# Performance work log

Measured on AMD Instinct MI355X. Metric: run time of the kernel, lower is better.

The kernel has to match this reference:

```python
import jax, jax.numpy as jnp
import numpy as np

N_QUBITS = 8
DEPTH = 2
DIM = 2 ** N_QUBITS

# Hadamard gate (symmetric)
_H = (1.0 / np.sqrt(2.0)) * jnp.array([[1.0, 1.0], [1.0, -1.0]], dtype=jnp.complex64)
# sign table for <Z_i>: bit of wire i is bit (n-1-i) of the basis index (wire 0 = MSB)
_bits = (np.arange(DIM)[:, None] >> np.arange(N_QUBITS - 1, -1, -1)[None, :]) & 1
_SIGNS = jnp.asarray(1.0 - 2.0 * _bits, dtype=jnp.float32)  # [DIM, n_qubits]


def _quantum(ang):
    """Vectorized statevector simulation of the circuit:
    RX(ang_i) on each wire, then DEPTH x (CNOT ladder + H on last wire);
    returns <Z_i> for each wire. ang: [R, N_QUBITS] float32 -> [R, N_QUBITS]."""
    R = ang.shape[0]
    half = ang * 0.5
    a0 = jnp.cos(half).astype(jnp.complex64)
    a1 = (jnp.sin(half) * (-1j)).astype(jnp.complex64)  # RX|0> = cos|0> - i sin|1>
    single = jnp.stack([a0, a1], axis=-1)  # [R, n, 2]
    # product state via kron over qubits (wire 0 is the most significant factor)
    state = single[:, 0]  # [R, 2]
    for q in range(1, N_QUBITS):
        state = (state[:, :, None] * single[:, q][:, None, :]).reshape(R, -1)
    for _ in range(DEPTH):
        # CNOT ladder on adjacent wires (i -> i+1)
        for i in range(N_QUBITS - 1):
            s = state.reshape(R, 2 ** i, 2, 2, -1)  # [R, pre, ctrl, tgt, post]
            s = jnp.concatenate([s[:, :, :1], s[:, :, 1:, ::-1]], axis=2)
            state = s.reshape(R, -1)
        # Hadamard on the last wire
        s = state.reshape(R, -1, 2)
        state = (s @ _H).reshape(R, -1)
    probs = state.real ** 2 + state.imag ** 2  # [R, DIM]
    return probs @ _SIGNS  # [R, n_qubits]


def setup_inputs() -> dict:
    key = jax.random.key(0)
    k_x, k_w1, k_w2 = jax.random.split(key, 3)
    B, S, E, F = 8, 4096, 1024, N_QUBITS
    x = jax.random.normal(k_x, (B, S, E), dtype=jnp.float32)
    w1 = jax.random.normal(k_w1, (F, E), dtype=jnp.float32) * 0.02
    b1 = jnp.zeros((F,), dtype=jnp.float32)
    w2 = jax.random.normal(k_w2, (E, F), dtype=jnp.float32) * 0.02
    b2 = jnp.zeros((E,), dtype=jnp.float32)
    return {"x": x, "w1": w1, "b1": b1, "w2": w2, "b2": b2}


def reference(x, w1, b1, w2, b2):
    B, S, E = x.shape
    h = jnp.einsum('bse,fe->bsf', x, w1) + b1  # linear1 -> [B, S, ffn_dim]
    q = _quantum(h.reshape(-1, N_QUBITS)).reshape(B, S, N_QUBITS)
    # dropout is identity in eval mode
    return jnp.einsum('bsf,ef->bse', q, w2) + b2  # linear2 -> [B, S, E]
```

## Files before the change

### kernel.cpp

```cpp
#include <hip/hip_runtime.h>


typedef float f4 __attribute__((ext_vector_type(4)));

constexpr int THREADS = 256;
constexpr int TILE    = 32;
constexpr int RPI     = 4;
constexpr int NGROUP  = TILE / RPI;
constexpr int E       = 1024;
constexpr int R_TOTAL = 8 * 4096;

static_assert(TILE * 8 == THREADS, "phase 2 uses all threads");

__global__ __launch_bounds__(THREADS, 4)
void ffq_kernel(const float* __restrict__ x,
                const float* __restrict__ w1,
                const float* __restrict__ b1,
                const float* __restrict__ w2,
                const float* __restrict__ b2,
                float* __restrict__ out)
{
    __shared__ float part[TILE][33];
    __shared__ __align__(16) float qsh[TILE][8];
    __shared__ float b1s[8];

    const int t    = threadIdx.x;
    const int lane = t & 63;
    const int wid  = t >> 6;
    const int c0   = t * 4;

    if (t < 8) b1s[t] = b1[t];

    f4 w1r[8];
#pragma unroll
    for (int f = 0; f < 8; ++f)
        w1r[f] = *(const f4*)(w1 + f * E + c0);

    const int row0 = blockIdx.x * TILE;
    const float* xp = x + (size_t)row0 * E + c0;

    f4 cur[RPI];
#pragma unroll
    for (int r = 0; r < RPI; ++r)
        cur[r] = *(const f4*)(xp + (size_t)r * E);

#pragma unroll
    for (int g = 0; g < NGROUP; ++g) {
        f4 xc[RPI];
#pragma unroll
        for (int r = 0; r < RPI; ++r) xc[r] = cur[r];

        if (g + 1 < NGROUP) {
#pragma unroll
            for (int r = 0; r < RPI; ++r)
                cur[r] = *(const f4*)(xp + (size_t)((g + 1) * RPI + r) * E);
        }

        float h[RPI][8];
#pragma unroll
        for (int r = 0; r < RPI; ++r)
#pragma unroll
            for (int f = 0; f < 8; ++f)
                h[r][f] = xc[r].x * w1r[f].x + xc[r].y * w1r[f].y
                        + xc[r].z * w1r[f].z + xc[r].w * w1r[f].w;

        {   const bool hb = lane & 1;
#pragma unroll
            for (int r = 0; r < RPI; ++r) {
                float s0 = hb ? h[r][0] : h[r][4];
                float s1 = hb ? h[r][1] : h[r][5];
                float s2 = hb ? h[r][2] : h[r][6];
                float s3 = hb ? h[r][3] : h[r][7];
                s0 = __shfl_xor(s0, 1); s1 = __shfl_xor(s1, 1);
                s2 = __shfl_xor(s2, 1); s3 = __shfl_xor(s3, 1);
                h[r][0] = (hb ? h[r][4] : h[r][0]) + s0;
                h[r][1] = (hb ? h[r][5] : h[r][1]) + s1;
                h[r][2] = (hb ? h[r][6] : h[r][2]) + s2;
                h[r][3] = (hb ? h[r][7] : h[r][3]) + s3;
            }
        }
        {   const bool hb = lane & 2;
#pragma unroll
            for (int r = 0; r < RPI; ++r) {
                float s0 = hb ? h[r][0] : h[r][2];
                float s1 = hb ? h[r][1] : h[r][3];
                s0 = __shfl_xor(s0, 2); s1 = __shfl_xor(s1, 2);
                h[r][0] = (hb ? h[r][2] : h[r][0]) + s0;
                h[r][1] = (hb ? h[r][3] : h[r][1]) + s1;
            }
        }
        float v[RPI];
        {   const bool hb = lane & 4;
#pragma unroll
            for (int r = 0; r < RPI; ++r) {
                float s0 = hb ? h[r][0] : h[r][1];
                s0 = __shfl_xor(s0, 4);
                v[r] = (hb ? h[r][1] : h[r][0]) + s0;
            }
        }
#pragma unroll
        for (int r = 0; r < RPI; ++r) v[r] += __shfl_xor(v[r], 8);
#pragma unroll
        for (int r = 0; r < RPI; ++r) v[r] += __shfl_xor(v[r], 16);
#pragma unroll
        for (int r = 0; r < RPI; ++r) v[r] += __shfl_xor(v[r], 32);

        if (lane < 8) {
            const int f = ((lane & 1) << 2) | (lane & 2) | ((lane >> 2) & 1);
#pragma unroll
            for (int r = 0; r < RPI; ++r)
                part[g * RPI + r][f * 4 + wid] = v[r];
        }
    }
    __syncthreads();

    {
        const int r = t >> 3;
        const int f = t & 7;
        const float hq = part[r][f * 4 + 0] + part[r][f * 4 + 1]
                       + part[r][f * 4 + 2] + part[r][f * 4 + 3] + b1s[f];
        float p = __cosf(hq);
        float u = __shfl_up(p, 2, 8); if (f >= 2) p *= u;
        u = __shfl_up(p, 4, 8);       if (f >= 4) p *= u;
        const float p6 = __shfl(p, 6, 8);
        if (f == 7) p *= p6;
        qsh[r][f] = p;
    }

    float w2a[4][8];
#pragma unroll
    for (int j = 0; j < 4; ++j) {
        const f4 lo = *(const f4*)(w2 + (size_t)(c0 + j) * 8);
        const f4 hi = *(const f4*)(w2 + (size_t)(c0 + j) * 8 + 4);
        w2a[j][0] = lo.x; w2a[j][1] = lo.y; w2a[j][2] = lo.z; w2a[j][3] = lo.w;
        w2a[j][4] = hi.x; w2a[j][5] = hi.y; w2a[j][6] = hi.z; w2a[j][7] = hi.w;
    }
    const f4 b2v = *(const f4*)(b2 + c0);

    __syncthreads();

#pragma unroll
    for (int s = 0; s < TILE; ++s) {
        const f4 qlo = *(const f4*)(&qsh[s][0]);
        const f4 qhi = *(const f4*)(&qsh[s][4]);
        const float qv[8] = {qlo.x, qlo.y, qlo.z, qlo.w,
                             qhi.x, qhi.y, qhi.z, qhi.w};
        f4 o = b2v;
#pragma unroll
        for (int f = 0; f < 8; ++f) {
            o.x += qv[f] * w2a[0][f];
            o.y += qv[f] * w2a[1][f];
            o.z += qv[f] * w2a[2][f];
            o.w += qv[f] * w2a[3][f];
        }
        __builtin_nontemporal_store(o, (f4*)(out + (size_t)(row0 + s) * E + c0));
    }
}

extern "C" void kernel_launch(void* const* d_in, const int* in_sizes, int n_in,
                              void* d_out, int out_size, void* d_ws, size_t ws_size,
                              hipStream_t stream)
{
    const float* x  = (const float*)d_in[0];
    const float* w1 = (const float*)d_in[1];
    const float* b1 = (const float*)d_in[2];
    const float* w2 = (const float*)d_in[3];
    const float* b2 = (const float*)d_in[4];
    float* out = (float*)d_out;

    ffq_kernel<<<dim3(R_TOTAL / TILE), THREADS, 0, stream>>>(x, w1, b1, w2, b2, out);
}
```

Baseline: 241.8 us.

## Split fused kernel into separate q-compute and expand kernels

Splits the single fused kernel into two launches: one that reads x, does the linear1 reduction and the quantum product, and writes 8 values per row to a workspace buffer, and one that reads those values and writes the 1024-wide output. The aim is to stop each block from alternating between a long read phase and a long write phase, so read and write traffic can each stream through their own kernel, with smaller tiles and higher occupancy on the expand side. The cost is an extra launch and a small intermediate buffer round-trip. When the workspace is too small, the q values are staged in the output buffer, which the expand kernel then overwrites.

```diff
diff --git a/kernel.cpp b/kernel.cpp
--- a/kernel.cpp
+++ b/kernel.cpp
@@ -4,24 +4,23 @@
 typedef float f4 __attribute__((ext_vector_type(4)));
 
 constexpr int THREADS = 256;
-constexpr int TILE    = 32;
-constexpr int RPI     = 4;
-constexpr int NGROUP  = TILE / RPI;
 constexpr int E       = 1024;
 constexpr int R_TOTAL = 8 * 4096;
 
-static_assert(TILE * 8 == THREADS, "phase 2 uses all threads");
+constexpr int TILE_A  = 16;
+constexpr int RPI     = 4;
+constexpr int NGROUP  = TILE_A / RPI;
+
+constexpr int TILE_B  = 16;
 
 __global__ __launch_bounds__(THREADS, 4)
-void ffq_kernel(const float* __restrict__ x,
-                const float* __restrict__ w1,
-                const float* __restrict__ b1,
-                const float* __restrict__ w2,
-                const float* __restrict__ b2,
-                float* __restrict__ out)
+void ffq_qcompute(const float* __restrict__ x,
+                  const float* __restrict__ w1,
+                  const float* __restrict__ b1,
+                  float* __restrict__ qbuf,
+                  const int qstride)
 {
-    __shared__ float part[TILE][33];
-    __shared__ __align__(16) float qsh[TILE][8];
+    __shared__ float part[TILE_A][33];
     __shared__ float b1s[8];
 
     const int t    = threadIdx.x;
@@ -36,7 +35,7 @@
     for (int f = 0; f < 8; ++f)
         w1r[f] = *(const f4*)(w1 + f * E + c0);
 
-    const int row0 = blockIdx.x * TILE;
+    const int row0 = blockIdx.x * TILE_A;
     const float* xp = x + (size_t)row0 * E + c0;
 
     f4 cur[RPI];
@@ -114,7 +113,7 @@
     }
     __syncthreads();
 
-    {
+    if (t < TILE_A * 8) {
         const int r = t >> 3;
         const int f = t & 7;
         const float hq = part[r][f * 4 + 0] + part[r][f * 4 + 1]
@@ -124,8 +123,25 @@
         u = __shfl_up(p, 4, 8);       if (f >= 4) p *= u;
         const float p6 = __shfl(p, 6, 8);
         if (f == 7) p *= p6;
-        qsh[r][f] = p;
+        qbuf[(size_t)(row0 + r) * qstride + f] = p;
     }
+}
+
+__global__ __launch_bounds__(THREADS, 8)
+void ffq_expand(const float* __restrict__ qbuf,
+                const int qstride,
+                const float* __restrict__ w2,
+                const float* __restrict__ b2,
+                float* __restrict__ out)
+{
+    __shared__ __align__(16) float qsh[TILE_B][8];
+
+    const int t  = threadIdx.x;
+    const int c0 = t * 4;
+    const int row0 = blockIdx.x * TILE_B;
+
+    if (t < TILE_B * 8)
+        qsh[t >> 3][t & 7] = qbuf[(size_t)(row0 + (t >> 3)) * qstride + (t & 7)];
 
     float w2a[4][8];
 #pragma unroll
@@ -140,7 +156,7 @@
     __syncthreads();
 
 #pragma unroll
-    for (int s = 0; s < TILE; ++s) {
+    for (int s = 0; s < TILE_B; ++s) {
         const f4 qlo = *(const f4*)(&qsh[s][0]);
         const f4 qhi = *(const f4*)(&qsh[s][4]);
         const float qv[8] = {qlo.x, qlo.y, qlo.z, qlo.w,
@@ -168,5 +184,14 @@
     const float* b2 = (const float*)d_in[4];
     float* out = (float*)d_out;
 
-    ffq_kernel<<<dim3(R_TOTAL / TILE), THREADS, 0, stream>>>(x, w1, b1, w2, b2, out);
+    float* qbuf;
+    int qstride;
+    if (ws_size >= (size_t)R_TOTAL * 8 * sizeof(float)) {
+        qbuf = (float*)d_ws; qstride = 8;
+    } else {
+        qbuf = out; qstride = E;
+    }
+
+    ffq_qcompute<<<dim3(R_TOTAL / TILE_A), THREADS, 0, stream>>>(x, w1, b1, qbuf, qstride);
+    ffq_expand  <<<dim3(R_TOTAL / TILE_B), THREADS, 0, stream>>>(qbuf, qstride, w2, b2, out);
 }
```

Measured after the change: 244.8 us. No clear change (+1.3%).
